# Kernel tuning notes

Hardware: AMD Instinct MI355X
Metric: run time of the kernel (lower is better)

Reference implementation:

```python
import jax, jax.numpy as jnp
import numpy as np

EMBED_DIM = 1024
B, T = 4, 2048

def setup_inputs() -> dict:
    key = jax.random.key(0)
    ks = jax.random.split(key, 7)
    s = 1.0 / np.sqrt(EMBED_DIM)
    return {
        "x": jax.random.normal(ks[0], (B, T, EMBED_DIM), dtype=jnp.float32),
        "Wq": jax.random.uniform(ks[1], (EMBED_DIM, EMBED_DIM), jnp.float32, -s, s),
        "bq": jax.random.uniform(ks[2], (EMBED_DIM,), jnp.float32, -s, s),
        "Wk": jax.random.uniform(ks[3], (EMBED_DIM, EMBED_DIM), jnp.float32, -s, s),
        "bk": jax.random.uniform(ks[4], (EMBED_DIM,), jnp.float32, -s, s),
        "Wv": jax.random.uniform(ks[5], (EMBED_DIM, EMBED_DIM), jnp.float32, -s, s),
        "bv": jax.random.uniform(ks[6], (EMBED_DIM,), jnp.float32, -s, s),
    }

def reference(x, Wq, bq, Wk, bk, Wv, bv):
    Bsz, Tlen, C = x.shape
    # torch Linear: y = x @ W.T + b
    Q = jnp.einsum('btc,dc->btd', x, Wq) + bq
    K = jnp.einsum('btc,dc->btd', x, Wk) + bk
    V = jnp.einsum('btc,dc->btd', x, Wv) + bv
    score = jnp.einsum('bqd,bkd->bqk', Q, K) / jnp.sqrt(jnp.float32(C))
    causal = jnp.tril(jnp.ones((Tlen, Tlen), dtype=bool))  # [T,T]
    score = jnp.where(causal, score, -jnp.inf)
    att = jax.nn.softmax(score, axis=-1)
    return jnp.einsum('bqk,bkd->bqd', att, V)
```

## Files before the change

### kernel.cpp

```cpp
#include <hip/hip_runtime.h>


using u16 = unsigned short;
typedef __attribute__((ext_vector_type(8))) short short8;
typedef __attribute__((ext_vector_type(4))) float f32x4;

__device__ __forceinline__ u16 f2b(float f) {
  unsigned u = __builtin_bit_cast(unsigned, f);
  u += 0x7fffu + ((u >> 16) & 1u);
  return (u16)(u >> 16);
}

__device__ __forceinline__ float b2f(u16 h) {
  return __builtin_bit_cast(float, (unsigned)h << 16);
}

__device__ __forceinline__ void async16(void* lds, const void* g) {
  __builtin_amdgcn_global_load_lds(
      (const __attribute__((address_space(1))) unsigned int*)g,
      (__attribute__((address_space(3))) unsigned int*)lds, 16, 0, 0);
}

__global__ __launch_bounds__(256) void cvt_kernel(const float* __restrict__ in,
                                                  u16* __restrict__ out, int n4) {
  const int i = blockIdx.x * 256 + threadIdx.x;
  if (i >= n4) return;
  const float4 v = reinterpret_cast<const float4*>(in)[i];
  ushort4 o;
  o.x = f2b(v.x); o.y = f2b(v.y); o.z = f2b(v.z); o.w = f2b(v.w);
  reinterpret_cast<ushort4*>(out)[i] = o;
}

__global__ __launch_bounds__(256) void cvt_w3_kernel(const float* __restrict__ Wq,
                                                     const float* __restrict__ Wk,
                                                     const float* __restrict__ Wv,
                                                     u16* __restrict__ Wcat) {
  const int bid = blockIdx.x;
  const int seg = bid >> 10;
  const int i = (bid & 1023) * 256 + threadIdx.x;
  const float* src = seg == 0 ? Wq : (seg == 1 ? Wk : Wv);
  const float4 v = reinterpret_cast<const float4*>(src)[i];
  ushort4 o;
  o.x = f2b(v.x); o.y = f2b(v.y); o.z = f2b(v.z); o.w = f2b(v.w);
  reinterpret_cast<ushort4*>(Wcat + (size_t)seg * 1048576)[i] = o;
}

template <typename Epi>
__device__ __forceinline__ void gemm_bt_tile(const u16* __restrict__ A, int lda,
                                             const u16* __restrict__ B, int ldb,
                                             int ksteps, Epi&& epi) {
  __shared__ __align__(16) u16 As[128 * 32];
  __shared__ __align__(16) u16 Bs[128 * 32];
  const int tid = threadIdx.x;
  const int lane = tid & 63;
  const int w = tid >> 6;
  const int wr = (w >> 1) << 6;
  const int wc = (w & 1) << 6;

  f32x4 zero = {0.f, 0.f, 0.f, 0.f};
  f32x4 acc[4][4];
#pragma unroll
  for (int i = 0; i < 4; ++i)
#pragma unroll
    for (int j = 0; j < 4; ++j) acc[i][j] = zero;

  const int sr = tid >> 2;
  const int sc = (tid & 3) << 3;
  const u16* ga0 = A + (size_t)sr * lda + sc;
  const u16* ga1 = A + (size_t)(sr + 64) * lda + sc;
  const u16* gb0 = B + (size_t)sr * ldb + sc;
  const u16* gb1 = B + (size_t)(sr + 64) * ldb + sc;
  u16* la0 = As + tid * 8;
  u16* la1 = As + 2048 + tid * 8;
  u16* lb0 = Bs + tid * 8;
  u16* lb1 = Bs + 2048 + tid * 8;

  const int foff = (lane & 15) * 32 + (lane >> 4) * 8;
  const u16* fa = As + wr * 32 + foff;
  const u16* fb = Bs + wc * 32 + foff;

  for (int ks = 0; ks < ksteps; ++ks) {
    __syncthreads();
    async16(la0, ga0);
    async16(la1, ga1);
    async16(lb0, gb0);
    async16(lb1, gb1);
    ga0 += 32; ga1 += 32; gb0 += 32; gb1 += 32;
    __syncthreads();
    short8 af[4], bf8[4];
#pragma unroll
    for (int i = 0; i < 4; ++i) af[i] = *(const short8*)(fa + (i << 9));
#pragma unroll
    for (int j = 0; j < 4; ++j) bf8[j] = *(const short8*)(fb + (j << 9));
#pragma unroll
    for (int i = 0; i < 4; ++i)
#pragma unroll
      for (int j = 0; j < 4; ++j)
        acc[i][j] = __builtin_amdgcn_mfma_f32_16x16x32_bf16(af[i], bf8[j],
                                                            acc[i][j], 0, 0, 0);
  }
  epi(acc, wr, wc, lane);
}

__global__ __launch_bounds__(256) void qkv_kernel(
    const u16* __restrict__ xb, const u16* __restrict__ Wcat,
    const float* __restrict__ bq, const float* __restrict__ bk,
    const float* __restrict__ bv, u16* __restrict__ Qb, u16* __restrict__ Kb,
    u16* __restrict__ Vtb) {
  const int bid = blockIdx.x;
  const int z = bid >> 9;
  const int r = bid & 511;
  if (z < 2) {
    const int mt = r >> 3, nt = r & 7;
    const u16* W = Wcat + (size_t)z * 1048576;
    const float* bias = z ? bk : bq;
    u16* out = z ? Kb : Qb;
    const float scale = z ? 1.0f : 0.03125f;
    gemm_bt_tile(
        xb + (size_t)mt * 128 * 1024, 1024, W + (size_t)nt * 128 * 1024, 1024, 32,
        [&](f32x4(&acc)[4][4], int wr, int wc, int lane) {
          const int r0 = mt * 128 + wr + ((lane >> 4) << 2);
          const int c0 = nt * 128 + wc + (lane & 15);
#pragma unroll
          for (int i = 0; i < 4; ++i)
#pragma unroll
            for (int j = 0; j < 4; ++j) {
              const int col = c0 + j * 16;
              const float bb = bias[col];
#pragma unroll
              for (int rr = 0; rr < 4; ++rr)
                out[(size_t)(r0 + i * 16 + rr) * 1024 + col] =
                    f2b((acc[i][j][rr] + bb) * scale);
            }
        });
  } else {
    const int mt = r >> 6, nt = r & 63;
    const u16* Wvb = Wcat + (size_t)2 * 1048576;
    gemm_bt_tile(
        Wvb + (size_t)mt * 128 * 1024, 1024, xb + (size_t)nt * 128 * 1024, 1024, 32,
        [&](f32x4(&acc)[4][4], int wr, int wc, int lane) {
          const int r0 = mt * 128 + wr + ((lane >> 4) << 2);
          const int c0 = nt * 128 + wc + (lane & 15);
#pragma unroll
          for (int i = 0; i < 4; ++i)
#pragma unroll
            for (int rr = 0; rr < 4; ++rr) {
              const int row = r0 + i * 16 + rr;
              const float bb = bv[row];
#pragma unroll
              for (int j = 0; j < 4; ++j)
                Vtb[(size_t)row * 8192 + c0 + j * 16] = f2b(acc[i][j][rr] + bb);
            }
        });
  }
}

__global__ __launch_bounds__(256) void score_kernel(const u16* __restrict__ Qb,
                                                    const u16* __restrict__ Kb,
                                                    u16* __restrict__ S) {
  const int b = blockIdx.y;
  const int t = blockIdx.x;
  int qt = 0;
  while ((qt + 1) * (qt + 2) / 2 <= t) ++qt;
  const int kt = t - (qt * (qt + 1)) / 2;
  const u16* A = Qb + ((size_t)b * 2048 + qt * 128) * 1024;
  const u16* Bp = Kb + ((size_t)b * 2048 + kt * 128) * 1024;
  u16* Sb = S + (size_t)b * 2048 * 2048;
  gemm_bt_tile(A, 1024, Bp, 1024, 32,
               [&](f32x4(&acc)[4][4], int wr, int wc, int lane) {
                 const int r0 = qt * 128 + wr + ((lane >> 4) << 2);
                 const int c0 = kt * 128 + wc + (lane & 15);
#pragma unroll
                 for (int i = 0; i < 4; ++i)
#pragma unroll
                   for (int j = 0; j < 4; ++j)
#pragma unroll
                     for (int rr = 0; rr < 4; ++rr)
                       Sb[(size_t)(r0 + i * 16 + rr) * 2048 + c0 + j * 16] =
                           f2b(acc[i][j][rr]);
               });
}

__global__ __launch_bounds__(256) void softmax_kernel(const u16* __restrict__ S,
                                                      u16* __restrict__ P) {
  __shared__ float redm[4], reds[4];
  const int rowid = blockIdx.x;
  const int b = rowid >> 11;
  const int q = rowid & 2047;
  const u16* Srow = S + ((size_t)b * 2048 + q) * 2048;
  u16* Prow = P + ((size_t)b * 2048 + q) * 2048;
  const int L = q + 1;
  const int Lpad = ((q >> 7) + 1) << 7;
  const int tid = threadIdx.x;
  const int k0 = tid << 3;
  const bool active = k0 < Lpad;
  float v[8];
  float m = -1e30f;
  if (active) {
    const short8 s8 = *(const short8*)(Srow + k0);
#pragma unroll
    for (int j = 0; j < 8; ++j) {
      v[j] = (k0 + j < L) ? b2f((u16)s8[j]) : -1e30f;
      m = fmaxf(m, v[j]);
    }
  }
#pragma unroll
  for (int o = 32; o > 0; o >>= 1) m = fmaxf(m, __shfl_xor(m, o));
  if ((tid & 63) == 0) redm[tid >> 6] = m;
  __syncthreads();
  m = fmaxf(fmaxf(redm[0], redm[1]), fmaxf(redm[2], redm[3]));
  float s = 0.f;
  if (active) {
#pragma unroll
    for (int j = 0; j < 8; ++j) {
      const float e = (k0 + j < L) ? __expf(v[j] - m) : 0.f;
      v[j] = e;
      s += e;
    }
  }
#pragma unroll
  for (int o = 32; o > 0; o >>= 1) s += __shfl_xor(s, o);
  if ((tid & 63) == 0) reds[tid >> 6] = s;
  __syncthreads();
  s = reds[0] + reds[1] + reds[2] + reds[3];
  const float inv = 1.0f / s;
  if (active) {
    short8 o8;
#pragma unroll
    for (int j = 0; j < 8; ++j)
      o8[j] = (short)((k0 + j < L) ? f2b(v[j] * inv) : (u16)0);
    *(short8*)(Prow + k0) = o8;
  }
}

__global__ __launch_bounds__(256) void pv_kernel(const u16* __restrict__ P,
                                                 const u16* __restrict__ Vtb,
                                                 float* __restrict__ O) {
  const int bid = blockIdx.x;
  const int pair = bid >> 8;
  const int idx = bid & 255;
  const int hb = idx >> 7;
  const int qt_raw = (idx >> 3) & 15;
  const int dt = idx & 7;
  const int qt = pair ? (15 - qt_raw) : qt_raw;
  const int b = pair * 2 + hb;
  const u16* A = P + (size_t)b * 2048 * 2048 + (size_t)qt * 128 * 2048;
  const u16* Bp = Vtb + (size_t)dt * 128 * 8192 + b * 2048;
  float* Ob = O + (size_t)b * 2048 * 1024;
  gemm_bt_tile(A, 2048, Bp, 8192, (qt + 1) * 4,
               [&](f32x4(&acc)[4][4], int wr, int wc, int lane) {
                 const int r0 = qt * 128 + wr + ((lane >> 4) << 2);
                 const int c0 = dt * 128 + wc + (lane & 15);
#pragma unroll
                 for (int i = 0; i < 4; ++i)
#pragma unroll
                   for (int j = 0; j < 4; ++j)
#pragma unroll
                     for (int rr = 0; rr < 4; ++rr)
                       Ob[(size_t)(r0 + i * 16 + rr) * 1024 + c0 + j * 16] =
                           acc[i][j][rr];
               });
}

extern "C" void kernel_launch(void* const* d_in, const int* in_sizes, int n_in,
                              void* d_out, int out_size, void* d_ws, size_t ws_size,
                              hipStream_t stream) {
  const float* x = (const float*)d_in[0];
  const float* Wq = (const float*)d_in[1];
  const float* bq = (const float*)d_in[2];
  const float* Wk = (const float*)d_in[3];
  const float* bk = (const float*)d_in[4];
  const float* Wv = (const float*)d_in[5];
  const float* bv = (const float*)d_in[6];
  float* out = (float*)d_out;
  char* ws = (char*)d_ws;
  u16* Qb = (u16*)(ws);
  u16* Kb = (u16*)(ws + (16u << 20));
  u16* Vtb = (u16*)(ws + (32u << 20));
  u16* xb = (u16*)(ws + (48u << 20));
  u16* Wcat = (u16*)(ws + (64u << 20));
  u16* S = (u16*)(ws + (70u << 20));
  u16* P = (u16*)(ws + (134u << 20));

  cvt_kernel<<<8192, 256, 0, stream>>>(x, xb, (8192 * 1024) / 4);
  cvt_w3_kernel<<<3072, 256, 0, stream>>>(Wq, Wk, Wv, Wcat);
  qkv_kernel<<<1536, 256, 0, stream>>>(xb, Wcat, bq, bk, bv, Qb, Kb, Vtb);
  score_kernel<<<dim3(136, 4), 256, 0, stream>>>(Qb, Kb, S);
  softmax_kernel<<<8192, 256, 0, stream>>>(S, P);
  pv_kernel<<<512, 256, 0, stream>>>(P, Vtb, out);
}
```

Measured before the change: 179.2 us.

## Double GEMM K-tile to 64 with XOR-swizzled LDS and fuse conversion kernels

Result: faster. 170.0 us (-5.1%).

```diff
diff --git a/kernel.cpp b/kernel.cpp
--- a/kernel.cpp
+++ b/kernel.cpp
@@ -21,83 +21,88 @@
       (__attribute__((address_space(3))) unsigned int*)lds, 16, 0, 0);
 }
 
-__global__ __launch_bounds__(256) void cvt_kernel(const float* __restrict__ in,
-                                                  u16* __restrict__ out, int n4) {
+__global__ __launch_bounds__(256) void cvt_all_kernel(
+    const float* __restrict__ x, const float* __restrict__ Wq,
+    const float* __restrict__ Wk, const float* __restrict__ Wv,
+    u16* __restrict__ xb, u16* __restrict__ Wcat) {
   const int i = blockIdx.x * 256 + threadIdx.x;
-  if (i >= n4) return;
-  const float4 v = reinterpret_cast<const float4*>(in)[i];
+  const float* src;
+  u16* dst;
+  int c;
+  if (i < 2097152) {
+    src = x; dst = xb; c = i;
+  } else {
+    const int r = i - 2097152;
+    const int seg = r >> 18;
+    src = seg == 0 ? Wq : (seg == 1 ? Wk : Wv);
+    dst = Wcat + (size_t)seg * 1048576;
+    c = r & 262143;
+  }
+  const float4 v = reinterpret_cast<const float4*>(src)[c];
   ushort4 o;
   o.x = f2b(v.x); o.y = f2b(v.y); o.z = f2b(v.z); o.w = f2b(v.w);
-  reinterpret_cast<ushort4*>(out)[i] = o;
-}
-
-__global__ __launch_bounds__(256) void cvt_w3_kernel(const float* __restrict__ Wq,
-                                                     const float* __restrict__ Wk,
-                                                     const float* __restrict__ Wv,
-                                                     u16* __restrict__ Wcat) {
-  const int bid = blockIdx.x;
-  const int seg = bid >> 10;
-  const int i = (bid & 1023) * 256 + threadIdx.x;
-  const float* src = seg == 0 ? Wq : (seg == 1 ? Wk : Wv);
-  const float4 v = reinterpret_cast<const float4*>(src)[i];
-  ushort4 o;
-  o.x = f2b(v.x); o.y = f2b(v.y); o.z = f2b(v.z); o.w = f2b(v.w);
-  reinterpret_cast<ushort4*>(Wcat + (size_t)seg * 1048576)[i] = o;
+  reinterpret_cast<ushort4*>(dst)[c] = o;
 }
 
 template <typename Epi>
 __device__ __forceinline__ void gemm_bt_tile(const u16* __restrict__ A, int lda,
                                              const u16* __restrict__ B, int ldb,
-                                             int ksteps, Epi&& epi) {
-  __shared__ __align__(16) u16 As[128 * 32];
-  __shared__ __align__(16) u16 Bs[128 * 32];
+                                             int nt, Epi&& epi) {
+  __shared__ __align__(16) u16 As[128 * 64];
+  __shared__ __align__(16) u16 Bs[128 * 64];
   const int tid = threadIdx.x;
   const int lane = tid & 63;
   const int w = tid >> 6;
   const int wr = (w >> 1) << 6;
   const int wc = (w & 1) << 6;
 
-  f32x4 zero = {0.f, 0.f, 0.f, 0.f};
   f32x4 acc[4][4];
 #pragma unroll
   for (int i = 0; i < 4; ++i)
 #pragma unroll
-    for (int j = 0; j < 4; ++j) acc[i][j] = zero;
-
-  const int sr = tid >> 2;
-  const int sc = (tid & 3) << 3;
-  const u16* ga0 = A + (size_t)sr * lda + sc;
-  const u16* ga1 = A + (size_t)(sr + 64) * lda + sc;
-  const u16* gb0 = B + (size_t)sr * ldb + sc;
-  const u16* gb1 = B + (size_t)(sr + 64) * ldb + sc;
-  u16* la0 = As + tid * 8;
-  u16* la1 = As + 2048 + tid * 8;
-  u16* lb0 = Bs + tid * 8;
-  u16* lb1 = Bs + 2048 + tid * 8;
-
-  const int foff = (lane & 15) * 32 + (lane >> 4) * 8;
-  const u16* fa = As + wr * 32 + foff;
-  const u16* fb = Bs + wc * 32 + foff;
-
-  for (int ks = 0; ks < ksteps; ++ks) {
+    for (int j = 0; j < 4; ++j) acc[i][j] = f32x4{0.f, 0.f, 0.f, 0.f};
+
+  const int sr = tid >> 3;
+  const int ce = ((tid & 7) ^ (sr & 7)) << 3;
+  const u16* gA = A + (size_t)sr * lda + ce;
+  const u16* gB = B + (size_t)sr * ldb + ce;
+  u16* const dA = As + tid * 8;
+  u16* const dB = Bs + tid * 8;
+
+  const int hi = lane >> 4;
+  const int lo7 = lane & 7;
+  const int ra = (wr + (lane & 15)) << 6;
+  const int rb = (wc + (lane & 15)) << 6;
+  const int sk0 = (hi ^ lo7) << 3;
+  const int sk1 = ((4 + hi) ^ lo7) << 3;
+
+  for (int t = 0; t < nt; ++t) {
     __syncthreads();
-    async16(la0, ga0);
-    async16(la1, ga1);
-    async16(lb0, gb0);
-    async16(lb1, gb1);
-    ga0 += 32; ga1 += 32; gb0 += 32; gb1 += 32;
+#pragma unroll
+    for (int s = 0; s < 4; ++s) {
+      async16(dA + s * 2048, gA + (size_t)(s * 32) * lda);
+      async16(dB + s * 2048, gB + (size_t)(s * 32) * ldb);
+    }
+    gA += 64;
+    gB += 64;
     __syncthreads();
-    short8 af[4], bf8[4];
-#pragma unroll
-    for (int i = 0; i < 4; ++i) af[i] = *(const short8*)(fa + (i << 9));
-#pragma unroll
-    for (int j = 0; j < 4; ++j) bf8[j] = *(const short8*)(fb + (j << 9));
-#pragma unroll
-    for (int i = 0; i < 4; ++i)
+#pragma unroll
+    for (int kk = 0; kk < 2; ++kk) {
+      const int sk = kk ? sk1 : sk0;
+      short8 af[4], bf[4];
+#pragma unroll
+      for (int i = 0; i < 4; ++i)
+        af[i] = *(const short8*)(As + ra + i * 1024 + sk);
 #pragma unroll
       for (int j = 0; j < 4; ++j)
-        acc[i][j] = __builtin_amdgcn_mfma_f32_16x16x32_bf16(af[i], bf8[j],
-                                                            acc[i][j], 0, 0, 0);
+        bf[j] = *(const short8*)(Bs + rb + j * 1024 + sk);
+#pragma unroll
+      for (int i = 0; i < 4; ++i)
+#pragma unroll
+        for (int j = 0; j < 4; ++j)
+          acc[i][j] = __builtin_amdgcn_mfma_f32_16x16x32_bf16(af[i], bf[j],
+                                                              acc[i][j], 0, 0, 0);
+    }
   }
   epi(acc, wr, wc, lane);
 }
@@ -117,7 +122,7 @@
     u16* out = z ? Kb : Qb;
     const float scale = z ? 1.0f : 0.03125f;
     gemm_bt_tile(
-        xb + (size_t)mt * 128 * 1024, 1024, W + (size_t)nt * 128 * 1024, 1024, 32,
+        xb + (size_t)mt * 128 * 1024, 1024, W + (size_t)nt * 128 * 1024, 1024, 16,
         [&](f32x4(&acc)[4][4], int wr, int wc, int lane) {
           const int r0 = mt * 128 + wr + ((lane >> 4) << 2);
           const int c0 = nt * 128 + wc + (lane & 15);
@@ -137,7 +142,7 @@
     const int mt = r >> 6, nt = r & 63;
     const u16* Wvb = Wcat + (size_t)2 * 1048576;
     gemm_bt_tile(
-        Wvb + (size_t)mt * 128 * 1024, 1024, xb + (size_t)nt * 128 * 1024, 1024, 32,
+        Wvb + (size_t)mt * 128 * 1024, 1024, xb + (size_t)nt * 128 * 1024, 1024, 16,
         [&](f32x4(&acc)[4][4], int wr, int wc, int lane) {
           const int r0 = mt * 128 + wr + ((lane >> 4) << 2);
           const int c0 = nt * 128 + wc + (lane & 15);
@@ -166,7 +171,7 @@
   const u16* A = Qb + ((size_t)b * 2048 + qt * 128) * 1024;
   const u16* Bp = Kb + ((size_t)b * 2048 + kt * 128) * 1024;
   u16* Sb = S + (size_t)b * 2048 * 2048;
-  gemm_bt_tile(A, 1024, Bp, 1024, 32,
+  gemm_bt_tile(A, 1024, Bp, 1024, 16,
                [&](f32x4(&acc)[4][4], int wr, int wc, int lane) {
                  const int r0 = qt * 128 + wr + ((lane >> 4) << 2);
                  const int c0 = kt * 128 + wc + (lane & 15);
@@ -247,7 +252,7 @@
   const u16* A = P + (size_t)b * 2048 * 2048 + (size_t)qt * 128 * 2048;
   const u16* Bp = Vtb + (size_t)dt * 128 * 8192 + b * 2048;
   float* Ob = O + (size_t)b * 2048 * 1024;
-  gemm_bt_tile(A, 2048, Bp, 8192, (qt + 1) * 4,
+  gemm_bt_tile(A, 2048, Bp, 8192, (qt + 1) * 2,
                [&](f32x4(&acc)[4][4], int wr, int wc, int lane) {
                  const int r0 = qt * 128 + wr + ((lane >> 4) << 2);
                  const int c0 = dt * 128 + wc + (lane & 15);
@@ -282,8 +287,7 @@
   u16* S = (u16*)(ws + (70u << 20));
   u16* P = (u16*)(ws + (134u << 20));
 
-  cvt_kernel<<<8192, 256, 0, stream>>>(x, xb, (8192 * 1024) / 4);
-  cvt_w3_kernel<<<3072, 256, 0, stream>>>(Wq, Wk, Wv, Wcat);
+  cvt_all_kernel<<<11264, 256, 0, stream>>>(x, Wq, Wk, Wv, xb, Wcat);
   qkv_kernel<<<1536, 256, 0, stream>>>(xb, Wcat, bq, bk, bv, Qb, Kb, Vtb);
   score_kernel<<<dim3(136, 4), 256, 0, stream>>>(Qb, Kb, S);
   softmax_kernel<<<8192, 256, 0, stream>>>(S, P);
```
